# Kernel optimization log

Measured on AMD Instinct MI355X. Metric: run time of the kernel, lower is better.

## Reference

```python
import jax, jax.numpy as jnp
import numpy as np

NUM_NODES = 50000
NUM_EDGES = 800000
INPUT_DIM = 256
OUTPUT_DIM = 256
NUM_HEADS = 8
HEAD_DIM = OUTPUT_DIM // NUM_HEADS


def setup_inputs() -> dict:
    key = jax.random.key(0)
    ks = jax.random.split(key, 14)
    x = jax.random.normal(ks[0], (NUM_NODES, INPUT_DIM), dtype=jnp.float32)
    edge_index = jax.random.randint(ks[1], (2, NUM_EDGES), 0, NUM_NODES, dtype=jnp.int32)
    # timestamps in seconds over ~11.5 days so log1p(|dt|/3600) is informative
    edge_time = jax.random.uniform(ks[2], (NUM_EDGES,), dtype=jnp.float32) * 1e6
    node_time = jax.random.uniform(ks[3], (NUM_NODES,), dtype=jnp.float32) * 1e6
    s_in = 1.0 / np.sqrt(INPUT_DIM)
    s_out = 1.0 / np.sqrt(OUTPUT_DIM)
    s_t = 1.0 / np.sqrt(2.0)
    Wq = jax.random.uniform(ks[4], (INPUT_DIM, OUTPUT_DIM), jnp.float32, -s_in, s_in)
    bq = jax.random.uniform(ks[5], (OUTPUT_DIM,), jnp.float32, -s_in, s_in)
    Wk = jax.random.uniform(ks[6], (INPUT_DIM, OUTPUT_DIM), jnp.float32, -s_in, s_in)
    bk = jax.random.uniform(ks[7], (OUTPUT_DIM,), jnp.float32, -s_in, s_in)
    Wv = jax.random.uniform(ks[8], (INPUT_DIM, OUTPUT_DIM), jnp.float32, -s_in, s_in)
    bv = jax.random.uniform(ks[9], (OUTPUT_DIM,), jnp.float32, -s_in, s_in)
    Wt = jax.random.uniform(ks[10], (2, NUM_HEADS), jnp.float32, -s_t, s_t)
    bt = jax.random.uniform(ks[11], (NUM_HEADS,), jnp.float32, -s_t, s_t)
    Wo = jax.random.uniform(ks[12], (OUTPUT_DIM, OUTPUT_DIM), jnp.float32, -s_out, s_out)
    bo = jax.random.uniform(ks[13], (OUTPUT_DIM,), jnp.float32, -s_out, s_out)
    return {"x": x, "edge_index": edge_index, "edge_time": edge_time, "node_time": node_time,
            "Wq": Wq, "bq": bq, "Wk": Wk, "bk": bk, "Wv": Wv, "bv": bv,
            "Wt": Wt, "bt": bt, "Wo": Wo, "bo": bo}


def reference(x, edge_index, edge_time, node_time, Wq, bq, Wk, bk, Wv, bv, Wt, bt, Wo, bo):
    n = x.shape[0]
    q = (x @ Wq + bq).reshape(n, NUM_HEADS, HEAD_DIM)
    k = (x @ Wk + bk).reshape(n, NUM_HEADS, HEAD_DIM)
    v = (x @ Wv + bv).reshape(n, NUM_HEADS, HEAD_DIM)
    src, dst = edge_index[0], edge_index[1]
    # temporal features per edge
    time_diff = edge_time - node_time[dst]
    time_features = jnp.stack(
        [jnp.sign(time_diff), jnp.log1p(jnp.abs(time_diff) / 3600.0)], axis=-1)  # [E, 2]
    temporal_weights = time_features @ Wt + bt  # [E, H]
    scale = HEAD_DIM ** -0.5
    scores = jnp.einsum('ehd,ehd->eh', q[dst], k[src]) * scale + temporal_weights  # [E, H]
    # softmax over ALL edges per head (dim=0), as in the original
    alpha = jax.nn.softmax(scores, axis=0)  # [E, H]
    msg = alpha[..., None] * v[src]  # [E, H, D]
    out = jax.ops.segment_sum(msg, dst, num_segments=n)  # [N, H, D]
    out = out.reshape(n, OUTPUT_DIM)
    return out @ Wo + bo
```

## Files before the change

### kernel.cpp

```cpp
#include <hip/hip_runtime.h>
#include <hip/hip_bf16.h>

#define NUM_NODES 50000
#define NUM_EDGES 800000
#define NUM_HEADS 8
#define HEAD_DIM 32
#define SCAN_BLOCKS 49

typedef unsigned short ushort8 __attribute__((ext_vector_type(8)));
typedef float f32x4 __attribute__((ext_vector_type(4)));
typedef __bf16 bf16x8 __attribute__((ext_vector_type(8)));

union BF8 { ushort8 u; bf16x8 b; };

__device__ __forceinline__ unsigned float_to_key(float f) {
    int i = __float_as_int(f);
    return (i >= 0) ? ((unsigned)i | 0x80000000u) : ~(unsigned)i;
}
__device__ __forceinline__ float key_to_float(unsigned u) {
    unsigned b = (u & 0x80000000u) ? (u & 0x7fffffffu) : ~u;
    return __int_as_float((int)b);
}
__device__ __forceinline__ float bf2f(unsigned short u) {
    return __uint_as_float(((unsigned)u) << 16);
}
__device__ __forceinline__ unsigned short f2bf(float f) {
    unsigned u = __float_as_uint(f);
    unsigned r = (u + 0x7fffu + ((u >> 16) & 1u)) >> 16;
    return (unsigned short)r;
}

__global__ __launch_bounds__(256) void deg_kernel(const int* __restrict__ dst_idx, int* __restrict__ deg) {
    int e = blockIdx.x * 256 + threadIdx.x;
    if (e < NUM_EDGES) atomicAdd(&deg[dst_idx[e]], 1);
}

__global__ __launch_bounds__(1024) void scanA_kernel(
    const int* __restrict__ deg, int* __restrict__ offs, int* __restrict__ blocksum)
{
    __shared__ int buf[1024];
    int tid = threadIdx.x;
    int i = blockIdx.x * 1024 + tid;
    int v = (i < NUM_NODES) ? deg[i] : 0;
    buf[tid] = v;
    __syncthreads();
    for (int off = 1; off < 1024; off <<= 1) {
        int t = (tid >= off) ? buf[tid - off] : 0;
        __syncthreads();
        buf[tid] += t;
        __syncthreads();
    }
    if (i < NUM_NODES) offs[i] = buf[tid] - v;
    if (tid == 1023) blocksum[blockIdx.x] = buf[1023];
}

__global__ __launch_bounds__(64) void scanB_kernel(
    const int* __restrict__ blocksum, int* __restrict__ carry, int* __restrict__ offs)
{
    if (threadIdx.x == 0) {
        int acc = 0;
        for (int b = 0; b < SCAN_BLOCKS; b++) { carry[b] = acc; acc += blocksum[b]; }
        offs[NUM_NODES] = acc;
    }
}

__global__ __launch_bounds__(256) void scanC_kernel(
    int* __restrict__ offs, const int* __restrict__ carry, int* __restrict__ cursor)
{
    int i = blockIdx.x * 256 + threadIdx.x;
    if (i < NUM_NODES) {
        int v = offs[i] + carry[i >> 10];
        offs[i] = v;
        cursor[i] = v;
    }
}

__global__ __launch_bounds__(256) void fill2_kernel(
    const int* __restrict__ src_idx, const int* __restrict__ dst_idx,
    const float* __restrict__ edge_time, int* __restrict__ cursor,
    int* __restrict__ src_s, int* __restrict__ dst_s, float* __restrict__ et_s)
{
    int e = blockIdx.x * 256 + threadIdx.x;
    if (e < NUM_EDGES) {
        int d = dst_idx[e];
        int pos = atomicAdd(&cursor[d], 1);
        src_s[pos] = src_idx[e];
        dst_s[pos] = d;
        et_s[pos] = edge_time[e];
    }
}

__global__ __launch_bounds__(256) void wtrans_kernel(
    const float* __restrict__ Wq, const float* __restrict__ Wk,
    const float* __restrict__ Wv, const float* __restrict__ Wo,
    unsigned short* __restrict__ Wt)
{
    __shared__ float t[64][65];
    int nb = blockIdx.x * 64;
    int kb = blockIdx.y * 64;
    int g = nb >> 8;
    const float* W = (g == 0) ? Wq : (g == 1) ? Wk : (g == 2) ? Wv : Wo;
    int n0 = nb & 255;
    int tx = threadIdx.x & 63;
    int ty = threadIdx.x >> 6;
#pragma unroll
    for (int i = 0; i < 16; i++) {
        int k = i * 4 + ty;
        t[tx][k] = W[(size_t)(kb + k) * 256 + n0 + tx];
    }
    __syncthreads();
#pragma unroll
    for (int i = 0; i < 16; i++) {
        int n = i * 4 + ty;
        Wt[(size_t)(nb + n) * 256 + kb + tx] = f2bf(t[n][tx]);
    }
}

__global__ __launch_bounds__(256) void wpack_kernel(
    const unsigned short* __restrict__ Wt, unsigned short* __restrict__ Wpk)
{
    int gid = blockIdx.x * 256 + threadIdx.x;
    int lane = gid & 63;
    int fragidx = gid >> 6;
    int c2 = fragidx & 7;
    int nf = (fragidx >> 3) & 3;
    int cb = (fragidx >> 5) & 3;
    int g = fragidx >> 7;
    int l16 = lane & 15;
    int kg = lane >> 4;
    int n_col = g * 256 + cb * 64 + nf * 16 + l16;
    int k0 = c2 * 32 + kg * 8;
    ushort8 v = *(const ushort8*)(Wt + (size_t)n_col * 256 + k0);
    *(ushort8*)(Wpk + (size_t)gid * 8) = v;
}

__global__ __launch_bounds__(256) void gemm_qkv_mfma6(
    const float* __restrict__ A, int M,
    const unsigned short* __restrict__ Wpk,
    const float* __restrict__ b0, const float* __restrict__ b1, const float* __restrict__ b2,
    unsigned short* __restrict__ O0, unsigned short* __restrict__ O1, unsigned short* __restrict__ O2)
{
    __shared__ unsigned short As[64 * 256];
    int tid = threadIdx.x;
    int rowbase = blockIdx.x * 64;

    {
        int rsub = tid >> 6;
        int c4 = (tid & 63) * 4;
        int cchunk = (tid & 63) >> 1;
        int sub = (tid & 1);
#pragma unroll
        for (int it = 0; it < 16; it++) {
            int row = it * 4 + rsub;
            int grow = rowbase + row;
            float4 av = make_float4(0.f, 0.f, 0.f, 0.f);
            if (grow < M) av = *(const float4*)(A + (size_t)grow * 256 + c4);
            ushort4 o;
            o.x = f2bf(av.x); o.y = f2bf(av.y); o.z = f2bf(av.z); o.w = f2bf(av.w);
            unsigned byte = row * 512 + ((unsigned)(cchunk ^ (row & 7)) << 4) + sub * 8;
            *(ushort4*)((char*)As + byte) = o;
        }
    }
    __syncthreads();

    int lane = tid & 63;
    int wid = tid >> 6;
    int l16 = lane & 15;
    int kg = lane >> 4;

#pragma unroll
    for (int p = 0; p < 3; p++) {
        const float* bias = (p == 0) ? b0 : (p == 1) ? b1 : b2;
        unsigned short* O = (p == 0) ? O0 : (p == 1) ? O1 : O2;

        f32x4 acc[4][4];
#pragma unroll
        for (int m = 0; m < 4; m++)
#pragma unroll
            for (int n = 0; n < 4; n++) acc[m][n] = (f32x4)(0.0f);

        const ushort8* wbase = (const ushort8*)(Wpk + ((size_t)(p * 4 + wid) * 2048 + lane) * 8);

#pragma unroll
        for (int c2 = 0; c2 < 8; c2++) {
            bf16x8 wfr[4];
#pragma unroll
            for (int n = 0; n < 4; n++) {
                BF8 t; t.u = wbase[(n * 8 + c2) * 64];
                wfr[n] = t.b;
            }
            bf16x8 afr[4];
#pragma unroll
            for (int m = 0; m < 4; m++) {
                int row = m * 16 + l16;
                int cchunk = (c2 * 4 + kg) ^ (row & 7);
                BF8 t;
                t.u = *(const ushort8*)((const char*)As + row * 512 + (cchunk << 4));
                afr[m] = t.b;
            }
#pragma unroll
            for (int m = 0; m < 4; m++)
#pragma unroll
                for (int n = 0; n < 4; n++)
                    acc[m][n] = __builtin_amdgcn_mfma_f32_16x16x32_bf16(wfr[n], afr[m], acc[m][n], 0, 0, 0);
        }

#pragma unroll
        for (int m = 0; m < 4; m++) {
            int node = rowbase + m * 16 + l16;
            if (node >= M) continue;
#pragma unroll
            for (int n = 0; n < 4; n++) {
                int lc = wid * 64 + n * 16 + kg * 4;
                float4 bv = *(const float4*)(bias + lc);
                ushort4 o;
                o.x = f2bf(acc[m][n][0] + bv.x);
                o.y = f2bf(acc[m][n][1] + bv.y);
                o.z = f2bf(acc[m][n][2] + bv.z);
                o.w = f2bf(acc[m][n][3] + bv.w);
                int hh = lc >> 5, dd = lc & 31;
                *(ushort4*)(O + ((size_t)hh * NUM_NODES + node) * 32 + dd) = o;
            }
        }
    }
}

__global__ __launch_bounds__(256) void gemm_out_mfma6(
    const unsigned short* __restrict__ aggb, int M,
    const unsigned short* __restrict__ Wpk,
    const float* __restrict__ bias, const float* __restrict__ kscale,
    float* __restrict__ C)
{
    __shared__ unsigned short As[64 * 256];
    int tid = threadIdx.x;
    int rowbase = blockIdx.x * 64;

    {
        int rsub = tid >> 6;
        int c4 = (tid & 63) * 4;
        int cchunk = (tid & 63) >> 1;
        int sub = (tid & 1);
        int hh = c4 >> 5, dd = c4 & 31;
        float ks = kscale[hh];
#pragma unroll
        for (int it = 0; it < 16; it++) {
            int row = it * 4 + rsub;
            int grow = rowbase + row;
            ushort4 av = make_ushort4(0, 0, 0, 0);
            if (grow < M) av = *(const ushort4*)(aggb + ((size_t)hh * NUM_NODES + grow) * 32 + dd);
            ushort4 o;
            o.x = f2bf(bf2f(av.x) * ks); o.y = f2bf(bf2f(av.y) * ks);
            o.z = f2bf(bf2f(av.z) * ks); o.w = f2bf(bf2f(av.w) * ks);
            unsigned byte = row * 512 + ((unsigned)(cchunk ^ (row & 7)) << 4) + sub * 8;
            *(ushort4*)((char*)As + byte) = o;
        }
    }
    __syncthreads();

    int lane = tid & 63;
    int wid = tid >> 6;
    int l16 = lane & 15;
    int kg = lane >> 4;

    f32x4 acc[4][4];
#pragma unroll
    for (int m = 0; m < 4; m++)
#pragma unroll
        for (int n = 0; n < 4; n++) acc[m][n] = (f32x4)(0.0f);

    const ushort8* wbase = (const ushort8*)(Wpk + ((size_t)wid * 2048 + lane) * 8);

#pragma unroll
    for (int c2 = 0; c2 < 8; c2++) {
        bf16x8 wfr[4];
#pragma unroll
        for (int n = 0; n < 4; n++) {
            BF8 t; t.u = wbase[(n * 8 + c2) * 64];
            wfr[n] = t.b;
        }
        bf16x8 afr[4];
#pragma unroll
        for (int m = 0; m < 4; m++) {
            int row = m * 16 + l16;
            int cchunk = (c2 * 4 + kg) ^ (row & 7);
            BF8 t;
            t.u = *(const ushort8*)((const char*)As + row * 512 + (cchunk << 4));
            afr[m] = t.b;
        }
#pragma unroll
        for (int m = 0; m < 4; m++)
#pragma unroll
            for (int n = 0; n < 4; n++)
                acc[m][n] = __builtin_amdgcn_mfma_f32_16x16x32_bf16(wfr[n], afr[m], acc[m][n], 0, 0, 0);
    }

#pragma unroll
    for (int m = 0; m < 4; m++) {
        int node = rowbase + m * 16 + l16;
        if (node >= M) continue;
#pragma unroll
        for (int n = 0; n < 4; n++) {
            int col = wid * 64 + n * 16 + kg * 4;
            float4 bv = *(const float4*)(bias + col);
            float4 o;
            o.x = acc[m][n][0] + bv.x;
            o.y = acc[m][n][1] + bv.y;
            o.z = acc[m][n][2] + bv.z;
            o.w = acc[m][n][3] + bv.w;
            *(float4*)(C + (size_t)node * 256 + col) = o;
        }
    }
}

__global__ __launch_bounds__(256) void score3_kernel(
    const unsigned short* __restrict__ qh, const unsigned short* __restrict__ kh,
    const int* __restrict__ src_s, const int* __restrict__ dst_s,
    const float* __restrict__ et_s, const float* __restrict__ node_time,
    const float* __restrict__ Wt, const float* __restrict__ bt,
    float* __restrict__ scores, unsigned* __restrict__ partialmax)
{
    __shared__ unsigned sm;
    int tid = threadIdx.x;
    if (tid == 0) sm = 0u;
    __syncthreads();
    int h = blockIdx.x & 7;
    int blk = blockIdx.x >> 3;
    float wt0 = Wt[h], wt1 = Wt[8 + h], btv = bt[h];
    const unsigned short* qhh = qh + (size_t)h * NUM_NODES * 32;
    const unsigned short* khh = kh + (size_t)h * NUM_NODES * 32;
    float* sc_h = scores + (size_t)h * NUM_EDGES;
    unsigned mykey = 0u;
    for (int pos = blk * 256 + tid; pos < NUM_EDGES; pos += 128 * 256) {
        int s = src_s[pos], d = dst_s[pos];
        const ushort8* qp = (const ushort8*)(qhh + (size_t)d * 32);
        const ushort8* kp = (const ushort8*)(khh + (size_t)s * 32);
        float dotv = 0.f;
#pragma unroll
        for (int i = 0; i < 4; i++) {
            ushort8 a = qp[i], b = kp[i];
#pragma unroll
            for (int j = 0; j < 8; j++) dotv += bf2f(a[j]) * bf2f(b[j]);
        }
        float td = et_s[pos] - node_time[d];
        float tf0 = (td > 0.f) ? 1.f : ((td < 0.f) ? -1.f : 0.f);
        float tf1 = log1pf(fabsf(td) * (1.f / 3600.f));
        float sc = dotv * 0.17677669529663687f + (tf0 * wt0 + tf1 * wt1 + btv);
        sc_h[pos] = sc;
        unsigned kkey = float_to_key(sc);
        mykey = (kkey > mykey) ? kkey : mykey;
    }
#pragma unroll
    for (int off = 32; off > 0; off >>= 1) {
        unsigned o = __shfl_xor(mykey, off, 64);
        mykey = (o > mykey) ? o : mykey;
    }
    if ((tid & 63) == 0) atomicMax(&sm, mykey);
    __syncthreads();
    if (tid == 0) partialmax[blockIdx.x] = sm;
}

__global__ __launch_bounds__(256) void reduce_max2_kernel(
    const unsigned* __restrict__ partialmax, float* __restrict__ headmax)
{
    int tid = threadIdx.x;
    int h = tid >> 5, lane = tid & 31;
    unsigned m = 0u;
#pragma unroll
    for (int k = 0; k < 4; k++) {
        unsigned v = partialmax[(lane + 32 * k) * 8 + h];
        m = (v > m) ? v : m;
    }
    for (int off = 16; off > 0; off >>= 1) {
        unsigned o = __shfl_down(m, off, 32);
        m = (o > m) ? o : m;
    }
    if (lane == 0) headmax[h] = key_to_float(m);
}

__global__ __launch_bounds__(256) void pexp_kernel(
    const float* __restrict__ scores, const float* __restrict__ headmax,
    unsigned short* __restrict__ pb, float* __restrict__ partialsum)
{
    __shared__ float ssum;
    int tid = threadIdx.x;
    if (tid == 0) ssum = 0.f;
    __syncthreads();
    int h = blockIdx.x & 7;
    int blk = blockIdx.x >> 3;
    float m = headmax[h];
    const float* sc_h = scores + (size_t)h * NUM_EDGES;
    unsigned short* p_h = pb + (size_t)h * NUM_EDGES;
    float s = 0.f;
    for (int pos = blk * 256 + tid; pos < NUM_EDGES; pos += 128 * 256) {
        float p = __expf(sc_h[pos] - m);
        p_h[pos] = f2bf(p);
        s += p;
    }
#pragma unroll
    for (int off = 32; off > 0; off >>= 1) s += __shfl_xor(s, off, 64);
    if ((tid & 63) == 0) atomicAdd(&ssum, s);
    __syncthreads();
    if (tid == 0) partialsum[blockIdx.x] = ssum;
}

__global__ __launch_bounds__(256) void reduce_psum_kernel(
    const float* __restrict__ partialsum, float* __restrict__ headinv)
{
    int tid = threadIdx.x;
    int h = tid >> 5, lane = tid & 31;
    float s = 0.f;
#pragma unroll
    for (int k = 0; k < 4; k++) s += partialsum[(lane + 32 * k) * 8 + h];
    for (int off = 16; off > 0; off >>= 1) s += __shfl_down(s, off, 32);
    if (lane == 0) headinv[h] = 1.f / s;
}

__global__ __launch_bounds__(256) void aggregate6_kernel(
    const unsigned short* __restrict__ vh, const unsigned short* __restrict__ pb,
    const int* __restrict__ src_s, const int* __restrict__ offs,
    unsigned short* __restrict__ aggb)
{
    int tid = threadIdx.x;
    int h = blockIdx.x & 7;
    int chunk = blockIdx.x >> 3;
    int g = tid >> 3;
    int ln = tid & 7;
    int node = chunk * 32 + g;
    const unsigned short* p_h = pb + (size_t)h * NUM_EDGES;
    const unsigned short* vhh = vh + (size_t)h * NUM_NODES * 32;
    int start = 0, end = 0;
    if (node < NUM_NODES) { start = offs[node]; end = offs[node + 1]; }
    f32x4 a0 = (f32x4)(0.f), a1 = (f32x4)(0.f);
    int cb = start;
    for (; cb + 2 <= end; cb += 2) {
        int s0 = src_s[cb], s1 = src_s[cb + 1];
        float p0 = bf2f(p_h[cb]), p1 = bf2f(p_h[cb + 1]);
        ushort4 v0 = *(const ushort4*)(vhh + (size_t)s0 * 32 + ln * 4);
        ushort4 v1 = *(const ushort4*)(vhh + (size_t)s1 * 32 + ln * 4);
        a0[0] += p0 * bf2f(v0.x); a0[1] += p0 * bf2f(v0.y);
        a0[2] += p0 * bf2f(v0.z); a0[3] += p0 * bf2f(v0.w);
        a1[0] += p1 * bf2f(v1.x); a1[1] += p1 * bf2f(v1.y);
        a1[2] += p1 * bf2f(v1.z); a1[3] += p1 * bf2f(v1.w);
    }
    if (cb < end) {
        int s0 = src_s[cb];
        float p0 = bf2f(p_h[cb]);
        ushort4 v0 = *(const ushort4*)(vhh + (size_t)s0 * 32 + ln * 4);
        a0[0] += p0 * bf2f(v0.x); a0[1] += p0 * bf2f(v0.y);
        a0[2] += p0 * bf2f(v0.z); a0[3] += p0 * bf2f(v0.w);
    }
    if (node < NUM_NODES) {
        ushort4 o;
        o.x = f2bf(a0[0] + a1[0]); o.y = f2bf(a0[1] + a1[1]);
        o.z = f2bf(a0[2] + a1[2]); o.w = f2bf(a0[3] + a1[3]);
        *(ushort4*)(aggb + ((size_t)h * NUM_NODES + node) * 32 + ln * 4) = o;
    }
}

extern "C" void kernel_launch(void* const* d_in, const int* in_sizes, int n_in,
                              void* d_out, int out_size, void* d_ws, size_t ws_size,
                              hipStream_t stream) {
    const float* x = (const float*)d_in[0];
    const int* ei = (const int*)d_in[1];
    const int* src_idx = ei;
    const int* dst_idx = ei + NUM_EDGES;
    const float* edge_time = (const float*)d_in[2];
    const float* node_time = (const float*)d_in[3];
    const float* Wq = (const float*)d_in[4];  const float* bq = (const float*)d_in[5];
    const float* Wk = (const float*)d_in[6];  const float* bk = (const float*)d_in[7];
    const float* Wv = (const float*)d_in[8];  const float* bv = (const float*)d_in[9];
    const float* Wt = (const float*)d_in[10]; const float* bt = (const float*)d_in[11];
    const float* Wo = (const float*)d_in[12]; const float* bo = (const float*)d_in[13];
    float* out = (float*)d_out;

    char* w = (char*)d_ws;
    unsigned short* qb = (unsigned short*)w; w += (size_t)NUM_NODES * 256 * 2;
    unsigned short* kb = (unsigned short*)w; w += (size_t)NUM_NODES * 256 * 2;
    unsigned short* vb = (unsigned short*)w; w += (size_t)NUM_NODES * 256 * 2;
    float* scores = (float*)w;      w += (size_t)NUM_EDGES * 8 * 4;
    unsigned short* pb = (unsigned short*)w; w += (size_t)NUM_EDGES * 8 * 2;
    unsigned short* aggb = (unsigned short*)w; w += (size_t)NUM_NODES * 256 * 2;
    int* src_s = (int*)w;           w += (size_t)NUM_EDGES * 4;
    int* dst_s = (int*)w;           w += (size_t)NUM_EDGES * 4;
    float* et_s = (float*)w;        w += (size_t)NUM_EDGES * 4;
    int* deg = (int*)w;             w += (size_t)NUM_NODES * 4;
    int* offs = (int*)w;            w += (size_t)(NUM_NODES + 1) * 4;
    int* cursor = (int*)w;          w += (size_t)NUM_NODES * 4;
    unsigned* partialmax = (unsigned*)w; w += 1024 * 4;
    float* partialsum = (float*)w;  w += 1024 * 4;
    float* headmax = (float*)w;     w += 8 * 4;
    float* headinv = (float*)w;     w += 8 * 4;
    int* blocksum = (int*)w;        w += 64 * 4;
    int* bcarry = (int*)w;          w += 64 * 4;
    unsigned short* Wtb = (unsigned short*)w; w += (size_t)1024 * 256 * 2;
    unsigned short* Wpk = (unsigned short*)w; w += (size_t)1024 * 256 * 2;

    hipMemsetAsync(deg, 0, (size_t)NUM_NODES * 4, stream);

    dim3 gw(16, 4);
    wtrans_kernel<<<gw, 256, 0, stream>>>(Wq, Wk, Wv, Wo, Wtb);
    wpack_kernel<<<128, 256, 0, stream>>>(Wtb, Wpk);

    deg_kernel<<<(NUM_EDGES + 255) / 256, 256, 0, stream>>>(dst_idx, deg);
    scanA_kernel<<<SCAN_BLOCKS, 1024, 0, stream>>>(deg, offs, blocksum);
    scanB_kernel<<<1, 64, 0, stream>>>(blocksum, bcarry, offs);
    scanC_kernel<<<(NUM_NODES + 255) / 256, 256, 0, stream>>>(offs, bcarry, cursor);
    fill2_kernel<<<(NUM_EDGES + 255) / 256, 256, 0, stream>>>(src_idx, dst_idx, edge_time,
                                                              cursor, src_s, dst_s, et_s);

    gemm_qkv_mfma6<<<(NUM_NODES + 63) / 64, 256, 0, stream>>>(
        x, NUM_NODES, Wpk, bq, bk, bv, qb, kb, vb);

    score3_kernel<<<1024, 256, 0, stream>>>(qb, kb, src_s, dst_s, et_s, node_time,
                                            Wt, bt, scores, partialmax);
    reduce_max2_kernel<<<1, 256, 0, stream>>>(partialmax, headmax);

    pexp_kernel<<<1024, 256, 0, stream>>>(scores, headmax, pb, partialsum);
    reduce_psum_kernel<<<1, 256, 0, stream>>>(partialsum, headinv);

    aggregate6_kernel<<<((NUM_NODES + 31) / 32) * 8, 256, 0, stream>>>(
        vb, pb, src_s, offs, aggb);

    gemm_out_mfma6<<<(NUM_NODES + 63) / 64, 256, 0, stream>>>(
        aggb, NUM_NODES, Wpk + (size_t)768 * 256, bo, headinv, out);
}
```

Before: 347.5 us.

## Fuse softmax exp and partial sums into the aggregation kernel

Removes the separate pexp pass that wrote bf16 probabilities to global memory. The aggregation kernel now stages each block's contiguous edge range (source indices plus exp of score minus max) in shared memory, accumulates per-head partial sums, and writes them per block for a new reduction kernel. This saves one kernel launch and a full write and read of the probability array. In exchange it adds block-wide syncs and a reduction over many more partials, and it reads fp32 scores instead of bf16 probabilities.

```diff
diff --git a/kernel.cpp b/kernel.cpp
--- a/kernel.cpp
+++ b/kernel.cpp
@@ -6,6 +6,7 @@
 #define NUM_HEADS 8
 #define HEAD_DIM 32
 #define SCAN_BLOCKS 49
+#define NCHUNK32 1563
 
 typedef unsigned short ushort8 __attribute__((ext_vector_type(8)));
 typedef float f32x4 __attribute__((ext_vector_type(4)));
@@ -377,84 +378,93 @@
     if (lane == 0) headmax[h] = key_to_float(m);
 }
 
-__global__ __launch_bounds__(256) void pexp_kernel(
-    const float* __restrict__ scores, const float* __restrict__ headmax,
-    unsigned short* __restrict__ pb, float* __restrict__ partialsum)
-{
-    __shared__ float ssum;
-    int tid = threadIdx.x;
-    if (tid == 0) ssum = 0.f;
-    __syncthreads();
+__global__ __launch_bounds__(256) void aggregate7_kernel(
+    const unsigned short* __restrict__ vh, const float* __restrict__ scores,
+    const int* __restrict__ src_s, const int* __restrict__ offs,
+    const float* __restrict__ headmax, unsigned short* __restrict__ aggb,
+    float* __restrict__ psum_part)
+{
+    __shared__ int sSrc[512];
+    __shared__ float sP[512];
+    __shared__ float blocksum;
+    int tid = threadIdx.x;
     int h = blockIdx.x & 7;
-    int blk = blockIdx.x >> 3;
+    int chunk = blockIdx.x >> 3;
+    int nodebase = chunk * 32;
+    int g = tid >> 3;
+    int ln = tid & 7;
+    int node = nodebase + g;
     float m = headmax[h];
     const float* sc_h = scores + (size_t)h * NUM_EDGES;
-    unsigned short* p_h = pb + (size_t)h * NUM_EDGES;
-    float s = 0.f;
-    for (int pos = blk * 256 + tid; pos < NUM_EDGES; pos += 128 * 256) {
-        float p = __expf(sc_h[pos] - m);
-        p_h[pos] = f2bf(p);
-        s += p;
-    }
-#pragma unroll
-    for (int off = 32; off > 0; off >>= 1) s += __shfl_xor(s, off, 64);
-    if ((tid & 63) == 0) atomicAdd(&ssum, s);
-    __syncthreads();
-    if (tid == 0) partialsum[blockIdx.x] = ssum;
-}
-
-__global__ __launch_bounds__(256) void reduce_psum_kernel(
-    const float* __restrict__ partialsum, float* __restrict__ headinv)
-{
-    int tid = threadIdx.x;
-    int h = tid >> 5, lane = tid & 31;
-    float s = 0.f;
-#pragma unroll
-    for (int k = 0; k < 4; k++) s += partialsum[(lane + 32 * k) * 8 + h];
-    for (int off = 16; off > 0; off >>= 1) s += __shfl_down(s, off, 32);
-    if (lane == 0) headinv[h] = 1.f / s;
-}
-
-__global__ __launch_bounds__(256) void aggregate6_kernel(
-    const unsigned short* __restrict__ vh, const unsigned short* __restrict__ pb,
-    const int* __restrict__ src_s, const int* __restrict__ offs,
-    unsigned short* __restrict__ aggb)
-{
-    int tid = threadIdx.x;
-    int h = blockIdx.x & 7;
-    int chunk = blockIdx.x >> 3;
-    int g = tid >> 3;
-    int ln = tid & 7;
-    int node = chunk * 32 + g;
-    const unsigned short* p_h = pb + (size_t)h * NUM_EDGES;
     const unsigned short* vhh = vh + (size_t)h * NUM_NODES * 32;
+    if (tid == 0) blocksum = 0.f;
+
+    int blkstart = offs[nodebase];
+    int blkend = offs[(nodebase + 32 < NUM_NODES) ? (nodebase + 32) : NUM_NODES];
     int start = 0, end = 0;
     if (node < NUM_NODES) { start = offs[node]; end = offs[node + 1]; }
+
     f32x4 a0 = (f32x4)(0.f), a1 = (f32x4)(0.f);
-    int cb = start;
-    for (; cb + 2 <= end; cb += 2) {
-        int s0 = src_s[cb], s1 = src_s[cb + 1];
-        float p0 = bf2f(p_h[cb]), p1 = bf2f(p_h[cb + 1]);
-        ushort4 v0 = *(const ushort4*)(vhh + (size_t)s0 * 32 + ln * 4);
-        ushort4 v1 = *(const ushort4*)(vhh + (size_t)s1 * 32 + ln * 4);
-        a0[0] += p0 * bf2f(v0.x); a0[1] += p0 * bf2f(v0.y);
-        a0[2] += p0 * bf2f(v0.z); a0[3] += p0 * bf2f(v0.w);
-        a1[0] += p1 * bf2f(v1.x); a1[1] += p1 * bf2f(v1.y);
-        a1[2] += p1 * bf2f(v1.z); a1[3] += p1 * bf2f(v1.w);
-    }
-    if (cb < end) {
-        int s0 = src_s[cb];
-        float p0 = bf2f(p_h[cb]);
-        ushort4 v0 = *(const ushort4*)(vhh + (size_t)s0 * 32 + ln * 4);
-        a0[0] += p0 * bf2f(v0.x); a0[1] += p0 * bf2f(v0.y);
-        a0[2] += p0 * bf2f(v0.z); a0[3] += p0 * bf2f(v0.w);
-    }
+    float ps = 0.f;
+
+    for (int t0 = blkstart; t0 < blkend; t0 += 512) {
+        int cnt = min(512, blkend - t0);
+        __syncthreads();
+        for (int i = tid; i < cnt; i += 256) {
+            sSrc[i] = src_s[t0 + i];
+            float p = __expf(sc_h[t0 + i] - m);
+            sP[i] = p;
+            ps += p;
+        }
+        __syncthreads();
+        int lo = (start > t0) ? start : t0;
+        int hi = (end < t0 + cnt) ? end : (t0 + cnt);
+        int cb = lo;
+        for (; cb + 2 <= hi; cb += 2) {
+            int i0 = cb - t0;
+            int s0 = sSrc[i0], s1 = sSrc[i0 + 1];
+            float p0 = sP[i0], p1 = sP[i0 + 1];
+            ushort4 v0 = *(const ushort4*)(vhh + (size_t)s0 * 32 + ln * 4);
+            ushort4 v1 = *(const ushort4*)(vhh + (size_t)s1 * 32 + ln * 4);
+            a0[0] += p0 * bf2f(v0.x); a0[1] += p0 * bf2f(v0.y);
+            a0[2] += p0 * bf2f(v0.z); a0[3] += p0 * bf2f(v0.w);
+            a1[0] += p1 * bf2f(v1.x); a1[1] += p1 * bf2f(v1.y);
+            a1[2] += p1 * bf2f(v1.z); a1[3] += p1 * bf2f(v1.w);
+        }
+        if (cb < hi) {
+            int i0 = cb - t0;
+            int s0 = sSrc[i0];
+            float p0 = sP[i0];
+            ushort4 v0 = *(const ushort4*)(vhh + (size_t)s0 * 32 + ln * 4);
+            a0[0] += p0 * bf2f(v0.x); a0[1] += p0 * bf2f(v0.y);
+            a0[2] += p0 * bf2f(v0.z); a0[3] += p0 * bf2f(v0.w);
+        }
+    }
+
     if (node < NUM_NODES) {
         ushort4 o;
         o.x = f2bf(a0[0] + a1[0]); o.y = f2bf(a0[1] + a1[1]);
         o.z = f2bf(a0[2] + a1[2]); o.w = f2bf(a0[3] + a1[3]);
         *(ushort4*)(aggb + ((size_t)h * NUM_NODES + node) * 32 + ln * 4) = o;
     }
+
+    __syncthreads();
+#pragma unroll
+    for (int off = 32; off > 0; off >>= 1) ps += __shfl_xor(ps, off, 64);
+    if ((tid & 63) == 0) atomicAdd(&blocksum, ps);
+    __syncthreads();
+    if (tid == 0) psum_part[blockIdx.x] = blocksum;
+}
+
+__global__ __launch_bounds__(256) void reduce_psum2_kernel(
+    const float* __restrict__ psum_part, float* __restrict__ headinv)
+{
+    int tid = threadIdx.x;
+    int h = tid >> 5, lane = tid & 31;
+    float s = 0.f;
+    for (int i = lane; i < NCHUNK32; i += 32) s += psum_part[i * 8 + h];
+    for (int off = 16; off > 0; off >>= 1) s += __shfl_down(s, off, 32);
+    if (lane == 0) headinv[h] = 1.f / s;
 }
 
 extern "C" void kernel_launch(void* const* d_in, const int* in_sizes, int n_in,
@@ -478,7 +488,6 @@
     unsigned short* kb = (unsigned short*)w; w += (size_t)NUM_NODES * 256 * 2;
     unsigned short* vb = (unsigned short*)w; w += (size_t)NUM_NODES * 256 * 2;
     float* scores = (float*)w;      w += (size_t)NUM_EDGES * 8 * 4;
-    unsigned short* pb = (unsigned short*)w; w += (size_t)NUM_EDGES * 8 * 2;
     unsigned short* aggb = (unsigned short*)w; w += (size_t)NUM_NODES * 256 * 2;
     int* src_s = (int*)w;           w += (size_t)NUM_EDGES * 4;
     int* dst_s = (int*)w;           w += (size_t)NUM_EDGES * 4;
@@ -487,7 +496,7 @@
     int* offs = (int*)w;            w += (size_t)(NUM_NODES + 1) * 4;
     int* cursor = (int*)w;          w += (size_t)NUM_NODES * 4;
     unsigned* partialmax = (unsigned*)w; w += 1024 * 4;
-    float* partialsum = (float*)w;  w += 1024 * 4;
+    float* psum_part = (float*)w;   w += (size_t)NCHUNK32 * 8 * 4;
     float* headmax = (float*)w;     w += 8 * 4;
     float* headinv = (float*)w;     w += 8 * 4;
     int* blocksum = (int*)w;        w += 64 * 4;
@@ -515,11 +524,9 @@
                                             Wt, bt, scores, partialmax);
     reduce_max2_kernel<<<1, 256, 0, stream>>>(partialmax, headmax);
 
-    pexp_kernel<<<1024, 256, 0, stream>>>(scores, headmax, pb, partialsum);
-    reduce_psum_kernel<<<1, 256, 0, stream>>>(partialsum, headinv);
-
-    aggregate6_kernel<<<((NUM_NODES + 31) / 32) * 8, 256, 0, stream>>>(
-        vb, pb, src_s, offs, aggb);
+    aggregate7_kernel<<<NCHUNK32 * 8, 256, 0, stream>>>(
+        vb, scores, src_s, offs, headmax, aggb, psum_part);
+    reduce_psum2_kernel<<<1, 256, 0, stream>>>(psum_part, headinv);
 
     gemm_out_mfma6<<<(NUM_NODES + 63) / 64, 256, 0, stream>>>(
         aggb, NUM_NODES, Wpk + (size_t)768 * 256, bo, headinv, out);
```

Measured after the change: 331.4 us. 1.05x faster.
